# Kernel tuning notes

Measured on AMD Instinct MI355X. Metric: run time of the kernel, lower is better.

## Reference

```python
import jax, jax.numpy as jnp
from jax import lax
import numpy as np

B, T, H, H2 = 2048, 512, 64, 16


def setup_inputs() -> dict:
    key = jax.random.key(0)
    ks = jax.random.split(key, 10)
    s_ih = 1.0 / np.sqrt(1 + 4 * H)   # xavier-ish scale for W_ih [4H, 1]
    s_hh = 1.0 / np.sqrt(H)
    return {
        "x":     jax.random.normal(ks[0], (B, T, 1), dtype=jnp.float32),
        "W_ih":  jax.random.normal(ks[1], (4 * H, 1), dtype=jnp.float32) * s_ih,
        "W_hh":  jax.random.normal(ks[2], (4 * H, H), dtype=jnp.float32) * s_hh,
        "b_ih":  jnp.zeros((4 * H,), dtype=jnp.float32),
        "b_hh":  jnp.zeros((4 * H,), dtype=jnp.float32),
        "fc1_w": jax.random.normal(ks[3], (H2, H), dtype=jnp.float32) * (1.0 / np.sqrt(H)),
        "fc1_b": jnp.zeros((H2,), dtype=jnp.float32),
        "fc2_w": jax.random.normal(ks[4], (1, H2), dtype=jnp.float32) * (1.0 / np.sqrt(H2)),
        "fc2_b": jnp.zeros((1,), dtype=jnp.float32),
    }


def _lstm_last_h(x, W_ih, W_hh, b_ih, b_hh):
    # PyTorch gate order: i, f, g, o. Precompute input projection for all steps.
    gx = jnp.einsum('bti,gi->btg', x, W_ih) + b_ih + b_hh  # [B, T, 4H]
    h0 = jnp.zeros((x.shape[0], W_hh.shape[1]), dtype=x.dtype)
    c0 = jnp.zeros_like(h0)

    def step(carry, g_t):
        h, c = carry
        g = g_t + h @ W_hh.T                       # [B, 4H]
        i, f, gc, o = jnp.split(g, 4, axis=-1)
        i = jax.nn.sigmoid(i)
        f = jax.nn.sigmoid(f)
        gc = jnp.tanh(gc)
        o = jax.nn.sigmoid(o)
        c = f * c + i * gc
        h = o * jnp.tanh(c)
        return (h, c), None

    (h, _), _ = lax.scan(step, (h0, c0), jnp.swapaxes(gx, 0, 1))  # scan over T
    return h  # [B, H] == out[:, -1, :]


def reference(x, W_ih, W_hh, b_ih, b_hh, fc1_w, fc1_b, fc2_w, fc2_b):
    h = _lstm_last_h(x, W_ih, W_hh, b_ih, b_hh)
    # dropout is identity in eval mode
    z = jax.nn.relu(h @ fc1_w.T + fc1_b)
    return z @ fc2_w.T + fc2_b  # [B, 1]
```

## Files before the change

### kernel.cpp

```cpp
#include <hip/hip_runtime.h>

namespace {

typedef __attribute__((ext_vector_type(8))) short short8;
typedef __attribute__((ext_vector_type(4))) float floatx4;

constexpr int T    = 512;
constexpr int H    = 64;
constexpr int TPB  = 512;
constexpr int MB   = 8;
constexpr int HST  = 128;
constexpr int XSTR = 516;
constexpr int FSTR = 68;

constexpr int DPP_ROR8 = 0x128;

__device__ __forceinline__ ushort f2bf(float x) {
  unsigned u = __float_as_uint(x);
  unsigned r = u + 0x7fffu + ((u >> 16) & 1u);
  return (ushort)(r >> 16);
}
__device__ __forceinline__ float bf2f(ushort h) {
  return __uint_as_float(((unsigned)h) << 16);
}
__device__ __forceinline__ float fsig(float x) {
  return __builtin_amdgcn_rcpf(1.0f + __expf(-x));
}
__device__ __forceinline__ float ftanh(float x) {
  return fmaf(-2.0f, __builtin_amdgcn_rcpf(1.0f + __expf(2.0f * x)), 1.0f);
}
__device__ __forceinline__ float swz8(float v) {
  return __int_as_float(__builtin_amdgcn_update_dpp(
      0, __float_as_int(v), DPP_ROR8, 0xf, 0xf, true));
}

__global__ __launch_bounds__(TPB, 2)
void lstm_mfma(const float* __restrict__ xg,
               const float* __restrict__ W_ih,
               const float* __restrict__ W_hh,
               const float* __restrict__ b_ih,
               const float* __restrict__ b_hh,
               const float* __restrict__ fc1_w,
               const float* __restrict__ fc1_b,
               const float* __restrict__ fc2_w,
               const float* __restrict__ fc2_b,
               float* __restrict__ out)
{
  __shared__ __align__(16) ushort hA[MB * HST];
  __shared__ __align__(16) ushort hB[MB * HST];
  __shared__ __align__(16) float  xs[MB * XSTR];
  __shared__ __align__(16) float  hf[MB * FSTR];
  __shared__ float zs[MB][16];

  const int tid  = threadIdx.x;
  const int b0   = blockIdx.x * MB;
  const int lane = tid & 63;
  const int wj   = tid >> 6;
  const int n    = lane & 15;
  const int kg   = lane >> 4;
  const int bat  = n & 7;
  const int nhi  = n >> 3;
  const int rot  = 24 * bat;

  for (int i = tid; i < MB * T / 4; i += TPB) {
    const int xb = i >> 7, tq = i & 127;
    float4 v = ((const float4*)(xg + (size_t)(b0 + xb) * T))[tq];
    *(float4*)&xs[xb * XSTR + tq * 4] = v;
  }
  for (int i = tid; i < MB * HST; i += TPB) { hA[i] = 0; hB[i] = 0; }

  short8 whi[2][2], wlo[2][2];
#pragma unroll
  for (int tt = 0; tt < 2; ++tt) {
    const int r    = 2 * wj + tt;
    const int arow = 64 * (n & 3) + 4 * r + (n >> 2);
    const float* wr = W_hh + arow * H + 8 * kg;
    const float4 p0 = *(const float4*)(wr + 0);
    const float4 p1 = *(const float4*)(wr + 4);
    const float4 p2 = *(const float4*)(wr + 32);
    const float4 p3 = *(const float4*)(wr + 36);
    const float v0[8] = {p0.x, p0.y, p0.z, p0.w, p1.x, p1.y, p1.z, p1.w};
    const float v1[8] = {p2.x, p2.y, p2.z, p2.w, p3.x, p3.y, p3.z, p3.w};
#pragma unroll
    for (int j = 0; j < 8; ++j) {
      const ushort h0 = f2bf(v0[j]);
      whi[tt][0][j] = (short)h0;
      wlo[tt][0][j] = (short)f2bf(v0[j] - bf2f(h0));
      const ushort h1 = f2bf(v1[j]);
      whi[tt][1][j] = (short)h1;
      wlo[tt][1][j] = (short)f2bf(v1[j] - bf2f(h1));
    }
  }

  const int u = 8 * wj + 4 * nhi + kg;
  float bia[4], wih[4];
#pragma unroll
  for (int j = 0; j < 4; ++j) {
    const int row = 64 * j + u;
    bia[j] = b_ih[row] + b_hh[row];
    wih[j] = W_ih[row];
  }

  const int Lrd   = 64 * nhi + 8 * kg;
  const int rd0   = bat * HST + ((Lrd      + rot) & 127);
  const int rd1   = bat * HST + ((Lrd + 32 + rot) & 127);
  const int whi_o = bat * HST + ((u        + rot) & 127);
  const int wlo_o = bat * HST + ((u + 64   + rot) & 127);
  const float* xq = &xs[bat * XSTR];
  float c = 0.0f, hk = 0.0f;

  __syncthreads();

#define STEP(HR, HW, XT)                                                       \
  {                                                                            \
    const short8 f0 = *(const short8*)((HR) + rd0);                            \
    const short8 f1 = *(const short8*)((HR) + rd1);                            \
    const floatx4 zf = {0.f, 0.f, 0.f, 0.f};                                   \
       \
        \
    floatx4 d = __builtin_amdgcn_mfma_f32_16x16x32_bf16(whi[0][0], f0, zf, 0, 0, 0); \
    floatx4 e = __builtin_amdgcn_mfma_f32_16x16x32_bf16(whi[1][0], f0, zf, 0, 0, 0); \
    d = __builtin_amdgcn_mfma_f32_16x16x32_bf16(wlo[0][0], f0, d, 0, 0, 0);    \
    e = __builtin_amdgcn_mfma_f32_16x16x32_bf16(wlo[1][0], f0, e, 0, 0, 0);    \
    d = __builtin_amdgcn_mfma_f32_16x16x32_bf16(whi[0][1], f1, d, 0, 0, 0);    \
    e = __builtin_amdgcn_mfma_f32_16x16x32_bf16(whi[1][1], f1, e, 0, 0, 0);    \
    d = __builtin_amdgcn_mfma_f32_16x16x32_bf16(wlo[0][1], f1, d, 0, 0, 0);    \
    e = __builtin_amdgcn_mfma_f32_16x16x32_bf16(wlo[1][1], f1, e, 0, 0, 0);    \
    float p[4];                                                                \
    _Pragma("unroll") for (int j = 0; j < 4; ++j) {                            \
      const float own  = nhi ? e[j] : d[j];       \
      const float send = nhi ? d[j] : e[j];       \
      p[j] = own + swz8(send) + fmaf((XT), wih[j], bia[j]);                    \
    }                                                                          \
    const float ig = fsig(p[0]);                                               \
    const float fg = fsig(p[1]);                                               \
    const float gc = ftanh(p[2]);                                              \
    const float og = fsig(p[3]);                                               \
    c  = fmaf(fg, c, ig * gc);                                                 \
    hk = og * ftanh(c);                                                        \
         \
    const ushort hib = (ushort)(__float_as_uint(hk) >> 16);                    \
    const float  rem = hk - bf2f(hib);                                         \
    (HW)[whi_o] = hib;                                                         \
    (HW)[wlo_o] = (ushort)(__float_as_uint(rem) >> 16);                        \
    __syncthreads();                                                           \
  }

  for (int t = 0; t < T; t += 2) {
    const float2 x2 = *(const float2*)(xq + t);
    STEP(hA, hB, x2.x);
    STEP(hB, hA, x2.y);
  }
#undef STEP

  hf[bat * FSTR + u] = hk;
  __syncthreads();
  if (tid < MB * 16) {
    const int bq = tid >> 4, j2 = tid & 15;
    float s = fc1_b[j2];
    const float* fw = fc1_w + j2 * H;
#pragma unroll
    for (int k = 0; k < H; ++k) s = fmaf(hf[bq * FSTR + k], fw[k], s);
    s = fmaxf(s, 0.0f);
    zs[bq][j2] = s * fc2_w[j2];
  }
  __syncthreads();
  if (tid < MB) {
    float s = fc2_b[0];
#pragma unroll
    for (int j = 0; j < 16; ++j) s += zs[tid][j];
    out[b0 + tid] = s;
  }
}

}

extern "C" void kernel_launch(void* const* d_in, const int* in_sizes, int n_in,
                              void* d_out, int out_size, void* d_ws, size_t ws_size,
                              hipStream_t stream) {
  const float* xg    = (const float*)d_in[0];
  const float* W_ih  = (const float*)d_in[1];
  const float* W_hh  = (const float*)d_in[2];
  const float* b_ih  = (const float*)d_in[3];
  const float* b_hh  = (const float*)d_in[4];
  const float* fc1_w = (const float*)d_in[5];
  const float* fc1_b = (const float*)d_in[6];
  const float* fc2_w = (const float*)d_in[7];
  const float* fc2_b = (const float*)d_in[8];
  float* out = (float*)d_out;

  dim3 grid(2048 / MB);
  dim3 block(TPB);
  hipLaunchKernelGGL(lstm_mfma, grid, block, 0, stream,
                     xg, W_ih, W_hh, b_ih, b_hh, fc1_w, fc1_b, fc2_w, fc2_b, out);
}
```

Measured before the change: 251.2 us.

## Halve batch per block and double MFMA tiles per wave

Each block now handles 4 sequences with 256 threads, and each wave computes four gate-row tiles instead of two, reducing the cross-lane reduction to DPP swizzles. This doubles the number of blocks and cuts per-step barrier participants, aiming to lower __syncthreads cost and improve latency hiding across the sequential time loop. The trade-off is twice as many MFMAs per wave per step and wasted MFMA columns, since only 4 batches fill the 16-wide N dimension.

```diff
diff --git a/kernel.cpp b/kernel.cpp
--- a/kernel.cpp
+++ b/kernel.cpp
@@ -7,8 +7,8 @@
 
 constexpr int T    = 512;
 constexpr int H    = 64;
-constexpr int TPB  = 512;
-constexpr int MB   = 8;
+constexpr int TPB  = 256;
+constexpr int MB   = 4;
 constexpr int HST  = 128;
 constexpr int XSTR = 516;
 constexpr int FSTR = 68;
@@ -58,8 +58,9 @@
   const int wj   = tid >> 6;
   const int n    = lane & 15;
   const int kg   = lane >> 4;
-  const int bat  = n & 7;
-  const int nhi  = n >> 3;
+  const int bat  = n & 3;
+  const int c2   = (n >> 2) & 1;
+  const int ty   = n >> 3;
   const int rot  = 24 * bat;
 
   for (int i = tid; i < MB * T / 4; i += TPB) {
@@ -69,10 +70,10 @@
   }
   for (int i = tid; i < MB * HST; i += TPB) { hA[i] = 0; hB[i] = 0; }
 
-  short8 whi[2][2], wlo[2][2];
-#pragma unroll
-  for (int tt = 0; tt < 2; ++tt) {
-    const int r    = 2 * wj + tt;
+  short8 whi[4][2], wlo[4][2];
+#pragma unroll
+  for (int tt = 0; tt < 4; ++tt) {
+    const int r    = 4 * wj + tt;
     const int arow = 64 * (n & 3) + 4 * r + (n >> 2);
     const float* wr = W_hh + arow * H + 8 * kg;
     const float4 p0 = *(const float4*)(wr + 0);
@@ -92,7 +93,7 @@
     }
   }
 
-  const int u = 8 * wj + 4 * nhi + kg;
+  const int u = 16 * wj + 4 * (n >> 2) + kg;
   float bia[4], wih[4];
 #pragma unroll
   for (int j = 0; j < 4; ++j) {
@@ -101,7 +102,7 @@
     wih[j] = W_ih[row];
   }
 
-  const int Lrd   = 64 * nhi + 8 * kg;
+  const int Lrd   = 64 * ty + 8 * kg;
   const int rd0   = bat * HST + ((Lrd      + rot) & 127);
   const int rd1   = bat * HST + ((Lrd + 32 + rot) & 127);
   const int whi_o = bat * HST + ((u        + rot) & 127);
@@ -116,21 +117,33 @@
     const short8 f0 = *(const short8*)((HR) + rd0);                            \
     const short8 f1 = *(const short8*)((HR) + rd1);                            \
     const floatx4 zf = {0.f, 0.f, 0.f, 0.f};                                   \
-       \
-        \
-    floatx4 d = __builtin_amdgcn_mfma_f32_16x16x32_bf16(whi[0][0], f0, zf, 0, 0, 0); \
-    floatx4 e = __builtin_amdgcn_mfma_f32_16x16x32_bf16(whi[1][0], f0, zf, 0, 0, 0); \
-    d = __builtin_amdgcn_mfma_f32_16x16x32_bf16(wlo[0][0], f0, d, 0, 0, 0);    \
-    e = __builtin_amdgcn_mfma_f32_16x16x32_bf16(wlo[1][0], f0, e, 0, 0, 0);    \
-    d = __builtin_amdgcn_mfma_f32_16x16x32_bf16(whi[0][1], f1, d, 0, 0, 0);    \
-    e = __builtin_amdgcn_mfma_f32_16x16x32_bf16(whi[1][1], f1, e, 0, 0, 0);    \
-    d = __builtin_amdgcn_mfma_f32_16x16x32_bf16(wlo[0][1], f1, d, 0, 0, 0);    \
-    e = __builtin_amdgcn_mfma_f32_16x16x32_bf16(wlo[1][1], f1, e, 0, 0, 0);    \
+      \
+    floatx4 a0 = __builtin_amdgcn_mfma_f32_16x16x32_bf16(whi[0][0], f0, zf, 0, 0, 0); \
+    floatx4 a1 = __builtin_amdgcn_mfma_f32_16x16x32_bf16(whi[1][0], f0, zf, 0, 0, 0); \
+    floatx4 a2 = __builtin_amdgcn_mfma_f32_16x16x32_bf16(whi[2][0], f0, zf, 0, 0, 0); \
+    floatx4 a3 = __builtin_amdgcn_mfma_f32_16x16x32_bf16(whi[3][0], f0, zf, 0, 0, 0); \
+    a0 = __builtin_amdgcn_mfma_f32_16x16x32_bf16(wlo[0][0], f0, a0, 0, 0, 0);  \
+    a1 = __builtin_amdgcn_mfma_f32_16x16x32_bf16(wlo[1][0], f0, a1, 0, 0, 0);  \
+    a2 = __builtin_amdgcn_mfma_f32_16x16x32_bf16(wlo[2][0], f0, a2, 0, 0, 0);  \
+    a3 = __builtin_amdgcn_mfma_f32_16x16x32_bf16(wlo[3][0], f0, a3, 0, 0, 0);  \
+    a0 = __builtin_amdgcn_mfma_f32_16x16x32_bf16(whi[0][1], f1, a0, 0, 0, 0);  \
+    a1 = __builtin_amdgcn_mfma_f32_16x16x32_bf16(whi[1][1], f1, a1, 0, 0, 0);  \
+    a2 = __builtin_amdgcn_mfma_f32_16x16x32_bf16(whi[2][1], f1, a2, 0, 0, 0);  \
+    a3 = __builtin_amdgcn_mfma_f32_16x16x32_bf16(whi[3][1], f1, a3, 0, 0, 0);  \
+    a0 = __builtin_amdgcn_mfma_f32_16x16x32_bf16(wlo[0][1], f1, a0, 0, 0, 0);  \
+    a1 = __builtin_amdgcn_mfma_f32_16x16x32_bf16(wlo[1][1], f1, a1, 0, 0, 0);  \
+    a2 = __builtin_amdgcn_mfma_f32_16x16x32_bf16(wlo[2][1], f1, a2, 0, 0, 0);  \
+    a3 = __builtin_amdgcn_mfma_f32_16x16x32_bf16(wlo[3][1], f1, a3, 0, 0, 0);  \
     float p[4];                                                                \
     _Pragma("unroll") for (int j = 0; j < 4; ++j) {                            \
-      const float own  = nhi ? e[j] : d[j];       \
-      const float send = nhi ? d[j] : e[j];       \
-      p[j] = own + swz8(send) + fmaf((XT), wih[j], bia[j]);                    \
+         \
+         \
+      const float m  = c2 ? a1[j] : a0[j];                                     \
+      const float q  = c2 ? a3[j] : a2[j];                                     \
+      const float sm = m + swz8(m);               \
+      const float sq = q + swz8(q);               \
+      const float own = ty ? sq : sm;                    \
+      p[j] = own + fmaf((XT), wih[j], bia[j]);                                 \
     }                                                                          \
     const float ig = fsig(p[0]);                                               \
     const float fg = fsig(p[1]);                                               \
```

Result: slower. 294.9 us (+17.4%).

## Double threads per block and split gate nonlinearities across lane halves

Applied to the files above, without the earlier changes.

Moves from 512 to 1024 threads per block so each wave handles one 16-row MFMA tile instead of two, halving the MFMA chain per step. The two lane halves split the four gate activations between them: one half computes input/output gates, the other forget/cell gates, exchanged via DPP swizzles. Each lane now writes either the hi or lo bf16 part of h, halving per-lane LDS stores. This shortens the serial per-timestep critical path, but the block-wide barrier now spans 16 waves and more DPP exchanges are added.

```diff
diff --git a/kernel.cpp b/kernel.cpp
--- a/kernel.cpp
+++ b/kernel.cpp
@@ -7,7 +7,7 @@
 
 constexpr int T    = 512;
 constexpr int H    = 64;
-constexpr int TPB  = 512;
+constexpr int TPB  = 1024;
 constexpr int MB   = 8;
 constexpr int HST  = 128;
 constexpr int XSTR = 516;
@@ -34,7 +34,7 @@
       0, __float_as_int(v), DPP_ROR8, 0xf, 0xf, true));
 }
 
-__global__ __launch_bounds__(TPB, 2)
+__global__ __launch_bounds__(TPB, 4)
 void lstm_mfma(const float* __restrict__ xg,
                const float* __restrict__ W_ih,
                const float* __restrict__ W_hh,
@@ -59,7 +59,7 @@
   const int n    = lane & 15;
   const int kg   = lane >> 4;
   const int bat  = n & 7;
-  const int nhi  = n >> 3;
+  const int ty   = n >> 3;
   const int rot  = 24 * bat;
 
   for (int i = tid; i < MB * T / 4; i += TPB) {
@@ -69,11 +69,9 @@
   }
   for (int i = tid; i < MB * HST; i += TPB) { hA[i] = 0; hB[i] = 0; }
 
-  short8 whi[2][2], wlo[2][2];
-#pragma unroll
-  for (int tt = 0; tt < 2; ++tt) {
-    const int r    = 2 * wj + tt;
-    const int arow = 64 * (n & 3) + 4 * r + (n >> 2);
+  short8 whi[2], wlo[2];
+  {
+    const int arow = 64 * (n & 3) + 4 * wj + (n >> 2);
     const float* wr = W_hh + arow * H + 8 * kg;
     const float4 p0 = *(const float4*)(wr + 0);
     const float4 p1 = *(const float4*)(wr + 4);
@@ -84,15 +82,15 @@
 #pragma unroll
     for (int j = 0; j < 8; ++j) {
       const ushort h0 = f2bf(v0[j]);
-      whi[tt][0][j] = (short)h0;
-      wlo[tt][0][j] = (short)f2bf(v0[j] - bf2f(h0));
+      whi[0][j] = (short)h0;
+      wlo[0][j] = (short)f2bf(v0[j] - bf2f(h0));
       const ushort h1 = f2bf(v1[j]);
-      whi[tt][1][j] = (short)h1;
-      wlo[tt][1][j] = (short)f2bf(v1[j] - bf2f(h1));
+      whi[1][j] = (short)h1;
+      wlo[1][j] = (short)f2bf(v1[j] - bf2f(h1));
     }
   }
 
-  const int u = 8 * wj + 4 * nhi + kg;
+  const int u = 4 * wj + kg;
   float bia[4], wih[4];
 #pragma unroll
   for (int j = 0; j < 4; ++j) {
@@ -101,13 +99,15 @@
     wih[j] = W_ih[row];
   }
 
-  const int Lrd   = 64 * nhi + 8 * kg;
-  const int rd0   = bat * HST + ((Lrd      + rot) & 127);
-  const int rd1   = bat * HST + ((Lrd + 32 + rot) & 127);
-  const int whi_o = bat * HST + ((u        + rot) & 127);
-  const int wlo_o = bat * HST + ((u + 64   + rot) & 127);
+  const float s2  = ty ? 2.0f : -1.0f;
+  const float mqb = ty ? -2.0f : 1.0f;
+  const float aqb = ty ? 1.0f : 0.0f;
+
+  const int rd0  = bat * HST + ((64 * ty + 8 * kg + rot) & 127);
+  const int rd1  = bat * HST + ((64 * ty + 8 * kg + 32 + rot) & 127);
+  const int wr_o = bat * HST + ((u + 64 * ty + rot) & 127);
   const float* xq = &xs[bat * XSTR];
-  float c = 0.0f, hk = 0.0f;
+  float c = 0.0f, hlast = 0.0f;
 
   __syncthreads();
 
@@ -116,33 +116,33 @@
     const short8 f0 = *(const short8*)((HR) + rd0);                            \
     const short8 f1 = *(const short8*)((HR) + rd1);                            \
     const floatx4 zf = {0.f, 0.f, 0.f, 0.f};                                   \
-       \
-        \
-    floatx4 d = __builtin_amdgcn_mfma_f32_16x16x32_bf16(whi[0][0], f0, zf, 0, 0, 0); \
-    floatx4 e = __builtin_amdgcn_mfma_f32_16x16x32_bf16(whi[1][0], f0, zf, 0, 0, 0); \
-    d = __builtin_amdgcn_mfma_f32_16x16x32_bf16(wlo[0][0], f0, d, 0, 0, 0);    \
-    e = __builtin_amdgcn_mfma_f32_16x16x32_bf16(wlo[1][0], f0, e, 0, 0, 0);    \
-    d = __builtin_amdgcn_mfma_f32_16x16x32_bf16(whi[0][1], f1, d, 0, 0, 0);    \
-    e = __builtin_amdgcn_mfma_f32_16x16x32_bf16(whi[1][1], f1, e, 0, 0, 0);    \
-    d = __builtin_amdgcn_mfma_f32_16x16x32_bf16(wlo[0][1], f1, d, 0, 0, 0);    \
-    e = __builtin_amdgcn_mfma_f32_16x16x32_bf16(wlo[1][1], f1, e, 0, 0, 0);    \
+              \
+    floatx4 d = __builtin_amdgcn_mfma_f32_16x16x32_bf16(whi[0], f0, zf, 0, 0, 0); \
+    d = __builtin_amdgcn_mfma_f32_16x16x32_bf16(wlo[0], f0, d, 0, 0, 0);       \
+    d = __builtin_amdgcn_mfma_f32_16x16x32_bf16(whi[1], f1, d, 0, 0, 0);       \
+    d = __builtin_amdgcn_mfma_f32_16x16x32_bf16(wlo[1], f1, d, 0, 0, 0);       \
     float p[4];                                                                \
     _Pragma("unroll") for (int j = 0; j < 4; ++j) {                            \
-      const float own  = nhi ? e[j] : d[j];       \
-      const float send = nhi ? d[j] : e[j];       \
-      p[j] = own + swz8(send) + fmaf((XT), wih[j], bia[j]);                    \
+          \
+      p[j] = d[j] + swz8(d[j]) + fmaf((XT), wih[j], bia[j]);                   \
     }                                                                          \
-    const float ig = fsig(p[0]);                                               \
-    const float fg = fsig(p[1]);                                               \
-    const float gc = ftanh(p[2]);                                              \
-    const float og = fsig(p[3]);                                               \
-    c  = fmaf(fg, c, ig * gc);                                                 \
-    hk = og * ftanh(c);                                                        \
-         \
-    const ushort hib = (ushort)(__float_as_uint(hk) >> 16);                    \
-    const float  rem = hk - bf2f(hib);                                         \
-    (HW)[whi_o] = hib;                                                         \
-    (HW)[wlo_o] = (ushort)(__float_as_uint(rem) >> 16);                        \
+     \
+    const float pa = ty ? p[3] : p[0];                                         \
+    const float pb = ty ? p[2] : p[1];                                         \
+    const float qa = fsig(pa);                                                 \
+    const float tb = __builtin_amdgcn_rcpf(1.0f + __expf(pb * s2));            \
+    const float qb = fmaf(mqb, tb, aqb);                                       \
+                       \
+    c = fmaf(qb, c, qa * swz8(qb));                                            \
+                       \
+    const float hk0 = swz8(qa) * ftanh(c);                                     \
+    const float hkx = swz8(hk0);                                               \
+    const float hku = ty ? hkx : hk0;                \
+    const ushort hib = (ushort)(__float_as_uint(hku) >> 16);     \
+    const float  rem = hku - bf2f(hib);                                        \
+    const ushort rus = (ushort)(__float_as_uint(rem) >> 16);     \
+    (HW)[wr_o] = ty ? rus : hib;                   \
+    hlast = hku;                                                               \
     __syncthreads();                                                           \
   }
 
@@ -153,7 +153,7 @@
   }
 #undef STEP
 
-  hf[bat * FSTR + u] = hk;
+  hf[bat * FSTR + u] = hlast;
   __syncthreads();
   if (tid < MB * 16) {
     const int bq = tid >> 4, j2 = tid & 15;
```

Measured after the change: 302.5 us. 20.4% more time.

## Process two independent batch groups per block to interleave recurrence chains

Applied to the files above, without the earlier changes.

Each block now handles 16 sequences as two independent groups of 8. Each step issues the MFMAs and gate math for both groups together, so one barrier covers both groups and the MFMA latency of one chain can overlap the other. The grid is halved to 128 blocks and registers and LDS per block grow. That risks leaving many CUs idle and lowering occupancy.

```diff
diff --git a/kernel.cpp b/kernel.cpp
--- a/kernel.cpp
+++ b/kernel.cpp
@@ -8,7 +8,8 @@
 constexpr int T    = 512;
 constexpr int H    = 64;
 constexpr int TPB  = 512;
-constexpr int MB   = 8;
+constexpr int MB   = 16;
+constexpr int SB   = 8;
 constexpr int HST  = 128;
 constexpr int XSTR = 516;
 constexpr int FSTR = 68;
@@ -46,8 +47,10 @@
                const float* __restrict__ fc2_b,
                float* __restrict__ out)
 {
-  __shared__ __align__(16) ushort hA[MB * HST];
-  __shared__ __align__(16) ushort hB[MB * HST];
+  __shared__ __align__(16) ushort hPA[SB * HST];
+  __shared__ __align__(16) ushort hPB[SB * HST];
+  __shared__ __align__(16) ushort hQA[SB * HST];
+  __shared__ __align__(16) ushort hQB[SB * HST];
   __shared__ __align__(16) float  xs[MB * XSTR];
   __shared__ __align__(16) float  hf[MB * FSTR];
   __shared__ float zs[MB][16];
@@ -67,7 +70,9 @@
     float4 v = ((const float4*)(xg + (size_t)(b0 + xb) * T))[tq];
     *(float4*)&xs[xb * XSTR + tq * 4] = v;
   }
-  for (int i = tid; i < MB * HST; i += TPB) { hA[i] = 0; hB[i] = 0; }
+  for (int i = tid; i < SB * HST; i += TPB) {
+    hPA[i] = 0; hPB[i] = 0; hQA[i] = 0; hQB[i] = 0;
+  }
 
   short8 whi[2][2], wlo[2][2];
 #pragma unroll
@@ -106,54 +111,78 @@
   const int rd1   = bat * HST + ((Lrd + 32 + rot) & 127);
   const int whi_o = bat * HST + ((u        + rot) & 127);
   const int wlo_o = bat * HST + ((u + 64   + rot) & 127);
-  const float* xq = &xs[bat * XSTR];
-  float c = 0.0f, hk = 0.0f;
+  const float* xqP = &xs[bat * XSTR];
+  const float* xqQ = &xs[(SB + bat) * XSTR];
+  float cP = 0.0f, hkP = 0.0f;
+  float cQ = 0.0f, hkQ = 0.0f;
 
   __syncthreads();
 
-#define STEP(HR, HW, XT)                                                       \
+#define STEP2(HRP, HWP, HRQ, HWQ, XTP, XTQ)                                    \
   {                                                                            \
-    const short8 f0 = *(const short8*)((HR) + rd0);                            \
-    const short8 f1 = *(const short8*)((HR) + rd1);                            \
+    const short8 f0p = *(const short8*)((HRP) + rd0);                          \
+    const short8 f1p = *(const short8*)((HRP) + rd1);                          \
+    const short8 f0q = *(const short8*)((HRQ) + rd0);                          \
+    const short8 f1q = *(const short8*)((HRQ) + rd1);                          \
     const floatx4 zf = {0.f, 0.f, 0.f, 0.f};                                   \
-       \
-        \
-    floatx4 d = __builtin_amdgcn_mfma_f32_16x16x32_bf16(whi[0][0], f0, zf, 0, 0, 0); \
-    floatx4 e = __builtin_amdgcn_mfma_f32_16x16x32_bf16(whi[1][0], f0, zf, 0, 0, 0); \
-    d = __builtin_amdgcn_mfma_f32_16x16x32_bf16(wlo[0][0], f0, d, 0, 0, 0);    \
-    e = __builtin_amdgcn_mfma_f32_16x16x32_bf16(wlo[1][0], f0, e, 0, 0, 0);    \
-    d = __builtin_amdgcn_mfma_f32_16x16x32_bf16(whi[0][1], f1, d, 0, 0, 0);    \
-    e = __builtin_amdgcn_mfma_f32_16x16x32_bf16(whi[1][1], f1, e, 0, 0, 0);    \
-    d = __builtin_amdgcn_mfma_f32_16x16x32_bf16(wlo[0][1], f1, d, 0, 0, 0);    \
-    e = __builtin_amdgcn_mfma_f32_16x16x32_bf16(wlo[1][1], f1, e, 0, 0, 0);    \
-    float p[4];                                                                \
+    floatx4 dp = __builtin_amdgcn_mfma_f32_16x16x32_bf16(whi[0][0], f0p, zf, 0, 0, 0); \
+    floatx4 ep = __builtin_amdgcn_mfma_f32_16x16x32_bf16(whi[1][0], f0p, zf, 0, 0, 0); \
+    floatx4 dq = __builtin_amdgcn_mfma_f32_16x16x32_bf16(whi[0][0], f0q, zf, 0, 0, 0); \
+    floatx4 eq = __builtin_amdgcn_mfma_f32_16x16x32_bf16(whi[1][0], f0q, zf, 0, 0, 0); \
+    dp = __builtin_amdgcn_mfma_f32_16x16x32_bf16(wlo[0][0], f0p, dp, 0, 0, 0); \
+    ep = __builtin_amdgcn_mfma_f32_16x16x32_bf16(wlo[1][0], f0p, ep, 0, 0, 0); \
+    dq = __builtin_amdgcn_mfma_f32_16x16x32_bf16(wlo[0][0], f0q, dq, 0, 0, 0); \
+    eq = __builtin_amdgcn_mfma_f32_16x16x32_bf16(wlo[1][0], f0q, eq, 0, 0, 0); \
+    dp = __builtin_amdgcn_mfma_f32_16x16x32_bf16(whi[0][1], f1p, dp, 0, 0, 0); \
+    ep = __builtin_amdgcn_mfma_f32_16x16x32_bf16(whi[1][1], f1p, ep, 0, 0, 0); \
+    dq = __builtin_amdgcn_mfma_f32_16x16x32_bf16(whi[0][1], f1q, dq, 0, 0, 0); \
+    eq = __builtin_amdgcn_mfma_f32_16x16x32_bf16(whi[1][1], f1q, eq, 0, 0, 0); \
+    dp = __builtin_amdgcn_mfma_f32_16x16x32_bf16(wlo[0][1], f1p, dp, 0, 0, 0); \
+    ep = __builtin_amdgcn_mfma_f32_16x16x32_bf16(wlo[1][1], f1p, ep, 0, 0, 0); \
+    dq = __builtin_amdgcn_mfma_f32_16x16x32_bf16(wlo[0][1], f1q, dq, 0, 0, 0); \
+    eq = __builtin_amdgcn_mfma_f32_16x16x32_bf16(wlo[1][1], f1q, eq, 0, 0, 0); \
+    float pp[4], pq[4];                                                        \
     _Pragma("unroll") for (int j = 0; j < 4; ++j) {                            \
-      const float own  = nhi ? e[j] : d[j];       \
-      const float send = nhi ? d[j] : e[j];       \
-      p[j] = own + swz8(send) + fmaf((XT), wih[j], bia[j]);                    \
+      const float ownp  = nhi ? ep[j] : dp[j];                                 \
+      const float sendp = nhi ? dp[j] : ep[j];                                 \
+      pp[j] = ownp + swz8(sendp) + fmaf((XTP), wih[j], bia[j]);                \
+      const float ownq  = nhi ? eq[j] : dq[j];                                 \
+      const float sendq = nhi ? dq[j] : eq[j];                                 \
+      pq[j] = ownq + swz8(sendq) + fmaf((XTQ), wih[j], bia[j]);                \
     }                                                                          \
-    const float ig = fsig(p[0]);                                               \
-    const float fg = fsig(p[1]);                                               \
-    const float gc = ftanh(p[2]);                                              \
-    const float og = fsig(p[3]);                                               \
-    c  = fmaf(fg, c, ig * gc);                                                 \
-    hk = og * ftanh(c);                                                        \
-         \
-    const ushort hib = (ushort)(__float_as_uint(hk) >> 16);                    \
-    const float  rem = hk - bf2f(hib);                                         \
-    (HW)[whi_o] = hib;                                                         \
-    (HW)[wlo_o] = (ushort)(__float_as_uint(rem) >> 16);                        \
+    const float igp = fsig(pp[0]);                                             \
+    const float fgp = fsig(pp[1]);                                             \
+    const float gcp = ftanh(pp[2]);                                            \
+    const float ogp = fsig(pp[3]);                                             \
+    cP  = fmaf(fgp, cP, igp * gcp);                                            \
+    hkP = ogp * ftanh(cP);                                                     \
+    const float igq = fsig(pq[0]);                                             \
+    const float fgq = fsig(pq[1]);                                             \
+    const float gcq = ftanh(pq[2]);                                            \
+    const float ogq = fsig(pq[3]);                                             \
+    cQ  = fmaf(fgq, cQ, igq * gcq);                                            \
+    hkQ = ogq * ftanh(cQ);                                                     \
+    const ushort hibp = (ushort)(__float_as_uint(hkP) >> 16);                  \
+    const float  remp = hkP - bf2f(hibp);                                      \
+    (HWP)[whi_o] = hibp;                                                       \
+    (HWP)[wlo_o] = (ushort)(__float_as_uint(remp) >> 16);                      \
+    const ushort hibq = (ushort)(__float_as_uint(hkQ) >> 16);                  \
+    const float  remq = hkQ - bf2f(hibq);                                      \
+    (HWQ)[whi_o] = hibq;                                                       \
+    (HWQ)[wlo_o] = (ushort)(__float_as_uint(remq) >> 16);                      \
     __syncthreads();                                                           \
   }
 
   for (int t = 0; t < T; t += 2) {
-    const float2 x2 = *(const float2*)(xq + t);
-    STEP(hA, hB, x2.x);
-    STEP(hB, hA, x2.y);
-  }
-#undef STEP
-
-  hf[bat * FSTR + u] = hk;
+    const float2 x2p = *(const float2*)(xqP + t);
+    const float2 x2q = *(const float2*)(xqQ + t);
+    STEP2(hPA, hPB, hQA, hQB, x2p.x, x2q.x);
+    STEP2(hPB, hPA, hQB, hQA, x2p.y, x2q.y);
+  }
+#undef STEP2
+
+  hf[bat * FSTR + u]        = hkP;
+  hf[(SB + bat) * FSTR + u] = hkQ;
   __syncthreads();
   if (tid < MB * 16) {
     const int bq = tid >> 4, j2 = tid & 15;
```

Result: slower. 400.1 us (+59.3%).
